# Optimization experiments

Hardware: AMD Instinct MI355X
Metric: run time of the kernel (lower is better)

The kernel has to match this reference:

```python
import jax, jax.numpy as jnp
import numpy as np

B, T, D, H = 2, 2048, 2048, 16


def setup_inputs() -> dict:
    key = jax.random.key(0)
    ks = jax.random.split(key, 5)
    s = 0.02  # typical init scale
    return {
        "x": jax.random.normal(ks[0], (B, T, D), jnp.float32),
        "wq": jax.random.normal(ks[1], (D, D), jnp.float32) * s,
        "wk": jax.random.normal(ks[2], (D, D), jnp.float32) * s,
        "wv": jax.random.normal(ks[3], (D, D), jnp.float32) * s,
        "wo": jax.random.normal(ks[4], (D, D), jnp.float32) * s,
    }


def weight_quant(w):
    # BitNet ternary-ish quant: sign(w) * mean(|w|), straight-through estimator
    scale = jnp.maximum(jnp.mean(jnp.abs(w)), 1e-5)
    q = jnp.sign(w) * scale
    return jax.lax.stop_gradient(q) + w - jax.lax.stop_gradient(w)


def reference(x, wq, wk, wv, wo):
    b, t, c = x.shape
    h = H
    hd = c // h
    # F.linear: y = x @ w.T  (weight shape [out, in])
    def proj(w):
        y = jnp.einsum('btc,dc->btd', x, weight_quant(w))
        return y.reshape(b, t, h, hd).transpose(0, 2, 1, 3)  # [b,h,t,hd]

    q, k, v = proj(wq), proj(wk), proj(wv)
    scale = 1.0 / np.sqrt(hd).astype(np.float32)
    scores = jnp.einsum('bhqd,bhkd->bhqk', q, k) * scale
    causal = jnp.tril(jnp.ones((t, t), dtype=bool))
    scores = jnp.where(causal, scores, jnp.finfo(scores.dtype).min)
    att = jax.nn.softmax(scores, axis=-1)
    y = jnp.einsum('bhqk,bhkd->bhqd', att, v)
    y = y.transpose(0, 2, 1, 3).reshape(b, t, c)
    return jnp.einsum('btc,dc->btd', y, weight_quant(wo))
```

## Files before the change

### kernel.cpp

```cpp
#include <hip/hip_runtime.h>
#include <stdint.h>

#define D_MODEL 2048
#define SEQ     2048
#define BATCH   2
#define NH      16
#define HD      128
#define M_TOT   (BATCH*SEQ)
#define NELEM_W (D_MODEL*D_MODEL)

typedef float f32x4 __attribute__((ext_vector_type(4)));
typedef short bf16x8 __attribute__((ext_vector_type(8)));

__device__ __forceinline__ unsigned short f2bf(float f) {
  union { float f; uint32_t u; } v; v.f = f;
  uint32_t r = v.u + 0x7FFFu + ((v.u >> 16) & 1u);
  return (unsigned short)(r >> 16);
}

__device__ __forceinline__ void gload_lds16(const unsigned short* g, unsigned short* l) {
  __builtin_amdgcn_global_load_lds(
      (const __attribute__((address_space(1))) unsigned int*)g,
      (__attribute__((address_space(3))) unsigned int*)l, 16, 0, 0);
}

__global__ __launch_bounds__(256) void sign_w(const float* w0, const float* w1,
                                              const float* w2, const float* w3,
                                              unsigned short* signs, float* partials) {
  const int wi = blockIdx.y;
  const float* w = (wi == 0) ? w0 : (wi == 1) ? w1 : (wi == 2) ? w2 : w3;
  unsigned short* o = signs + (size_t)wi * NELEM_W;
  const int t = threadIdx.x;
  const int i = blockIdx.x * 256 + t;
  float4 v = ((const float4*)w)[i];
  ushort4 s;
  s.x = (v.x > 0.f) ? 0x3F80u : ((v.x < 0.f) ? 0xBF80u : 0u);
  s.y = (v.y > 0.f) ? 0x3F80u : ((v.y < 0.f) ? 0xBF80u : 0u);
  s.z = (v.z > 0.f) ? 0x3F80u : ((v.z < 0.f) ? 0xBF80u : 0u);
  s.w = (v.w > 0.f) ? 0x3F80u : ((v.w < 0.f) ? 0xBF80u : 0u);
  ((ushort4*)o)[i] = s;
  float a = fabsf(v.x) + fabsf(v.y) + fabsf(v.z) + fabsf(v.w);
  #pragma unroll
  for (int off = 32; off; off >>= 1) a += __shfl_down(a, off);
  __shared__ float sm[4];
  if ((t & 63) == 0) sm[t >> 6] = a;
  __syncthreads();
  if (t == 0) partials[wi * 4096 + blockIdx.x] = sm[0] + sm[1] + sm[2] + sm[3];
}

__global__ __launch_bounds__(256) void reduce2(const float* partials, float* scales) {
  const int wi = blockIdx.x, t = threadIdx.x;
  float s = 0.f;
  #pragma unroll
  for (int i = 0; i < 16; ++i) s += partials[wi * 4096 + i * 256 + t];
  #pragma unroll
  for (int off = 32; off; off >>= 1) s += __shfl_down(s, off);
  __shared__ float sm[4];
  if ((t & 63) == 0) sm[t >> 6] = s;
  __syncthreads();
  if (t == 0) scales[wi] = fmaxf((sm[0] + sm[1] + sm[2] + sm[3]) * (1.f / 4194304.f), 1e-5f);
}

__global__ __launch_bounds__(256) void cvt_x(const float* x, unsigned short* xb) {
  const int i = blockIdx.x * 256 + threadIdx.x;
  float4 v = ((const float4*)x)[i];
  ushort4 o;
  o.x = f2bf(v.x); o.y = f2bf(v.y); o.z = f2bf(v.z); o.w = f2bf(v.w);
  ((ushort4*)xb)[i] = o;
}

template <int MODE>
__global__ __launch_bounds__(512, 2) void gemm_p(const unsigned short* __restrict__ A,
                                                 const unsigned short* __restrict__ W,
                                                 unsigned short* __restrict__ Qb,
                                                 unsigned short* __restrict__ Kb,
                                                 unsigned short* __restrict__ Vt,
                                                 float* __restrict__ outf,
                                                 const float* __restrict__ scales) {
  constexpr int K = 2048;
  constexpr int NT = K / 64;
  constexpr int BUF = 24576;
  __shared__ alignas(16) unsigned short lds[3 * BUF];
  const int t = threadIdx.x;
  const int wid = t >> 6, lane = t & 63;
  const int llo = lane & 15, lhi = lane >> 4;
  const int wm = wid >> 1, wn = wid & 1;

  const int nwg = gridDim.x;
  const int bid = blockIdx.x;
  const int sid = (bid & 7) * (nwg >> 3) + (bid >> 3);
  const int mt = sid & 15, nt_ = sid >> 4;
  const int m0 = mt * 256;
  const int n0w = nt_ * 128;

  auto stageA = [&](int buf, int kt, int half) {
    const int k0 = kt * 64;
    #pragma unroll
    for (int i = half * 2; i < half * 2 + 2; ++i) {
      const int c = i * 512 + t;
      const int row = c >> 3, slot = c & 7;
      gload_lds16(A + (size_t)(m0 + row) * K + k0 + ((slot ^ (row & 7)) << 3),
                  &lds[buf * BUF + (i * 512 + wid * 64) * 8]);
    }
  };
  auto stageB = [&](int buf, int kt) {
    const int k0 = kt * 64;
    #pragma unroll
    for (int i = 0; i < 2; ++i) {
      const int c = i * 512 + t;
      const int row = c >> 3, slot = c & 7;
      gload_lds16(W + (size_t)(n0w + row) * K + k0 + ((slot ^ (row & 7)) << 3),
                  &lds[buf * BUF + 16384 + (i * 512 + wid * 64) * 8]);
    }
  };

  f32x4 acc[4][4] = {};
  bf16x8 a[2][2], b0[2][2], b1[2][2];

  auto rdA = [&](int cur, int mh) {
    #pragma unroll
    for (int fm = 0; fm < 2; ++fm) {
      const int ra = wm * 64 + mh * 32 + fm * 16 + llo;
      #pragma unroll
      for (int kk = 0; kk < 2; ++kk)
        a[fm][kk] = *(const bf16x8*)&lds[cur * BUF + ra * 64 + (((kk * 4 + lhi) ^ (ra & 7)) << 3)];
    }
  };

  stageA(0, 0, 0); stageA(0, 0, 1); stageB(0, 0);
  stageA(1, 1, 0); stageA(1, 1, 1); stageB(1, 1);
  asm volatile("s_waitcnt vmcnt(6)" ::: "memory");
  __builtin_amdgcn_s_barrier();

  for (int kt = 0; kt < NT; ++kt) {
    const int cur = kt % 3;
    const int nb3 = (kt + 2) % 3;
    const bool pf = (kt + 2) < NT;
    rdA(cur, 0);
    #pragma unroll
    for (int fn = 0; fn < 2; ++fn) {
      const int rb = wn * 64 + fn * 16 + llo;
      #pragma unroll
      for (int kk = 0; kk < 2; ++kk)
        b0[fn][kk] = *(const bf16x8*)&lds[cur * BUF + 16384 + rb * 64 + (((kk * 4 + lhi) ^ (rb & 7)) << 3)];
    }
    if (pf) stageA(nb3, kt + 2, 0);
    __builtin_amdgcn_s_barrier();
    asm volatile("s_waitcnt lgkmcnt(0)" ::: "memory");
    __builtin_amdgcn_sched_barrier(0);
    __builtin_amdgcn_s_setprio(1);
    #pragma unroll
    for (int kk = 0; kk < 2; ++kk)
      #pragma unroll
      for (int fm = 0; fm < 2; ++fm)
        #pragma unroll
        for (int fn = 0; fn < 2; ++fn)
          acc[fm][fn] = __builtin_amdgcn_mfma_f32_16x16x32_bf16(a[fm][kk], b0[fn][kk], acc[fm][fn], 0, 0, 0);
    __builtin_amdgcn_s_setprio(0);
    __builtin_amdgcn_s_barrier();
    #pragma unroll
    for (int fn = 0; fn < 2; ++fn) {
      const int rb = wn * 64 + 32 + fn * 16 + llo;
      #pragma unroll
      for (int kk = 0; kk < 2; ++kk)
        b1[fn][kk] = *(const bf16x8*)&lds[cur * BUF + 16384 + rb * 64 + (((kk * 4 + lhi) ^ (rb & 7)) << 3)];
    }
    if (pf) stageA(nb3, kt + 2, 1);
    __builtin_amdgcn_s_barrier();
    asm volatile("s_waitcnt lgkmcnt(0)" ::: "memory");
    __builtin_amdgcn_sched_barrier(0);
    __builtin_amdgcn_s_setprio(1);
    #pragma unroll
    for (int kk = 0; kk < 2; ++kk)
      #pragma unroll
      for (int fm = 0; fm < 2; ++fm)
        #pragma unroll
        for (int fn = 0; fn < 2; ++fn)
          acc[fm][2 + fn] = __builtin_amdgcn_mfma_f32_16x16x32_bf16(a[fm][kk], b1[fn][kk], acc[fm][2 + fn], 0, 0, 0);
    __builtin_amdgcn_s_setprio(0);
    __builtin_amdgcn_s_barrier();
    rdA(cur, 1);
    if (pf) stageB(nb3, kt + 2);
    __builtin_amdgcn_s_barrier();
    asm volatile("s_waitcnt lgkmcnt(0)" ::: "memory");
    __builtin_amdgcn_sched_barrier(0);
    __builtin_amdgcn_s_setprio(1);
    #pragma unroll
    for (int kk = 0; kk < 2; ++kk)
      #pragma unroll
      for (int fm = 0; fm < 2; ++fm)
        #pragma unroll
        for (int fn = 0; fn < 2; ++fn)
          acc[2 + fm][2 + fn] = __builtin_amdgcn_mfma_f32_16x16x32_bf16(a[fm][kk], b1[fn][kk], acc[2 + fm][2 + fn], 0, 0, 0);
    __builtin_amdgcn_s_setprio(0);
    __builtin_amdgcn_s_barrier();
    if (pf) asm volatile("s_waitcnt vmcnt(6)" ::: "memory");
    else    asm volatile("s_waitcnt vmcnt(0)" ::: "memory");
    __builtin_amdgcn_s_barrier();
    __builtin_amdgcn_s_setprio(1);
    #pragma unroll
    for (int kk = 0; kk < 2; ++kk)
      #pragma unroll
      for (int fm = 0; fm < 2; ++fm)
        #pragma unroll
        for (int fn = 0; fn < 2; ++fn)
          acc[2 + fm][fn] = __builtin_amdgcn_mfma_f32_16x16x32_bf16(a[fm][kk], b0[fn][kk], acc[2 + fm][fn], 0, 0, 0);
    __builtin_amdgcn_s_setprio(0);
    __builtin_amdgcn_s_barrier();
  }

  if (MODE == 1) {
    const float sc = scales[3];
    #pragma unroll
    for (int fm = 0; fm < 4; ++fm)
      #pragma unroll
      for (int fn = 0; fn < 4; ++fn)
        #pragma unroll
        for (int r = 0; r < 4; ++r) {
          const int row = m0 + wm * 64 + fm * 16 + lhi * 4 + r;
          const int col = n0w + wn * 64 + fn * 16 + llo;
          outf[(size_t)row * D_MODEL + col] = acc[fm][fn][r] * sc;
        }
  } else {
    const int region = n0w >> 11;
    const int c0 = (n0w & 2047) + wn * 64;
    const float sc = scales[region] * (region == 0 ? 0.08838834764831845f : 1.f);
    unsigned short* outb = (region == 0) ? Qb : (region == 1) ? Kb : Vt;
    #pragma unroll
    for (int fm = 0; fm < 4; ++fm)
      #pragma unroll
      for (int fn = 0; fn < 4; ++fn)
        #pragma unroll
        for (int r = 0; r < 4; ++r) {
          const int row = m0 + wm * 64 + fm * 16 + lhi * 4 + r;
          const int colr = c0 + fn * 16 + llo;
          const int b = row >> 11, tt = row & 2047, h = colr >> 7, d = colr & 127;
          size_t idx;
          if (region < 2) idx = ((size_t)((b * NH + h) * SEQ + tt)) * HD + d;
          else            idx = ((size_t)((b * NH + h) * HD + d)) * SEQ + tt;
          outb[idx] = f2bf(acc[fm][fn][r] * sc);
        }
  }
}

__global__ __launch_bounds__(512, 4) void attn_fwd(const unsigned short* __restrict__ Q,
                                                   const unsigned short* __restrict__ Kt,
                                                   const unsigned short* __restrict__ VT,
                                                   unsigned short* __restrict__ O) {
  __shared__ alignas(16) unsigned short lds[2][16384];
  __shared__ alignas(16) unsigned short plds[8][1024];
  const int t = threadIdx.x;
  const int wid = t >> 6, lane = t & 63;
  const int llo = lane & 15, lhi = lane >> 4;
  const int j0 = blockIdx.x;
  int bh, g;
  if (j0 < 256) { bh = j0 & 31; g = 15 - (j0 >> 5); }
  else          { bh = (j0 - 256) & 31; g = (j0 - 256) >> 5; }
  const int qbase = g * 128;
  const int nt = 2 * g + 2;
  const size_t bh_td = (size_t)bh * SEQ * HD;
  const size_t bh_dt = (size_t)bh * HD * SEQ;
  unsigned short* pw = &plds[wid][0];
  const int fvl = (llo & 7) ^ ((llo & 8) >> 1);
  const int pkey = llo & 14;

  auto stage = [&](int buf, int j) {
    const int t0 = j * 64;
    #pragma unroll
    for (int i = 0; i < 2; ++i) {
      const int c = i * 512 + t;
      const int row = c >> 4, slot = c & 15;
      gload_lds16(Kt + bh_td + (size_t)(t0 + row) * HD + ((slot ^ (row & 15)) << 3),
                  &lds[buf][(size_t)(i * 512 + wid * 64) * 8]);
    }
    #pragma unroll
    for (int i = 0; i < 2; ++i) {
      const int c = i * 512 + t;
      const int vrow = c >> 3, vslot = c & 7;
      const int fv = (vrow & 7) ^ ((vrow & 8) >> 1);
      gload_lds16(VT + bh_dt + (size_t)vrow * SEQ + t0 + ((vslot ^ fv) << 3),
                  &lds[buf][8192 + (size_t)(i * 512 + wid * 64) * 8]);
    }
  };

  bf16x8 qa[4];
  {
    const unsigned short* qp = Q + bh_td + (size_t)(qbase + wid * 16 + llo) * HD + lhi * 8;
    #pragma unroll
    for (int kk = 0; kk < 4; ++kk) qa[kk] = *(const bf16x8*)(qp + kk * 32);
  }
  f32x4 oacc[8] = {};
  float m_r = -1e30f, l_r = 0.f;

  stage(0, 0);
  for (int j = 0; j < nt; ++j) {
    const int cur = j & 1;
    __syncthreads();
    if (j + 1 < nt) stage(cur ^ 1, j + 1);
    f32x4 s[4] = {};
    __builtin_amdgcn_s_setprio(1);
    #pragma unroll
    for (int nb = 0; nb < 4; ++nb) {
      const int row = nb * 16 + llo;
      #pragma unroll
      for (int kk = 0; kk < 4; ++kk) {
        const bf16x8 kb = *(const bf16x8*)&lds[cur][row * 128 + (((kk * 4 + lhi) ^ llo) << 3)];
        s[nb] = __builtin_amdgcn_mfma_f32_16x16x32_bf16(kb, qa[kk], s[nb], 0, 0, 0);
      }
    }
    __builtin_amdgcn_s_setprio(0);
    if (j >= nt - 2) {
      const int q = qbase + wid * 16 + llo;
      #pragma unroll
      for (int nb = 0; nb < 4; ++nb)
        #pragma unroll
        for (int r = 0; r < 4; ++r)
          if (j * 64 + nb * 16 + lhi * 4 + r > q) s[nb][r] = -1e30f;
    }
    float mloc = -1e30f;
    #pragma unroll
    for (int nb = 0; nb < 4; ++nb)
      #pragma unroll
      for (int r = 0; r < 4; ++r) mloc = fmaxf(mloc, s[nb][r]);
    mloc = fmaxf(mloc, __shfl_xor(mloc, 16));
    mloc = fmaxf(mloc, __shfl_xor(mloc, 32));
    float alq = 1.f;
    if (__any(mloc > m_r + 8.f)) {
      const float mn = fmaxf(m_r, mloc);
      alq = __expf(m_r - mn);
      m_r = mn;
      float alr[4];
      #pragma unroll
      for (int r = 0; r < 4; ++r) alr[r] = __shfl(alq, lhi * 4 + r);
      #pragma unroll
      for (int db = 0; db < 8; ++db)
        #pragma unroll
        for (int r = 0; r < 4; ++r) oacc[db][r] *= alr[r];
    }
    float ps = 0.f;
    #pragma unroll
    for (int nb = 0; nb < 4; ++nb) {
      const float p0 = __expf(s[nb][0] - m_r), p1 = __expf(s[nb][1] - m_r);
      const float p2 = __expf(s[nb][2] - m_r), p3 = __expf(s[nb][3] - m_r);
      ps += (p0 + p1) + (p2 + p3);
      uint2 uu;
      uu.x = (uint32_t)f2bf(p0) | ((uint32_t)f2bf(p1) << 16);
      uu.y = (uint32_t)f2bf(p2) | ((uint32_t)f2bf(p3) << 16);
      *(uint2*)&pw[llo * 64 + (((nb * 4 + lhi) ^ pkey) << 2)] = uu;
    }
    ps += __shfl_xor(ps, 16);
    ps += __shfl_xor(ps, 32);
    l_r = l_r * alq + ps;
    asm volatile("s_waitcnt lgkmcnt(0)" ::: "memory");
    __builtin_amdgcn_sched_barrier(0);
    const bf16x8 pa0 = *(const bf16x8*)&pw[llo * 64 + (((lhi * 2) ^ pkey) << 2)];
    const bf16x8 pa1 = *(const bf16x8*)&pw[llo * 64 + (((8 + lhi * 2) ^ pkey) << 2)];
    __builtin_amdgcn_s_setprio(1);
    #pragma unroll
    for (int db = 0; db < 8; ++db) {
      const unsigned short* vbp = &lds[cur][8192 + (db * 16 + llo) * 64];
      const bf16x8 vb0 = *(const bf16x8*)&vbp[(lhi ^ fvl) << 3];
      const bf16x8 vb1 = *(const bf16x8*)&vbp[((4 + lhi) ^ fvl) << 3];
      oacc[db] = __builtin_amdgcn_mfma_f32_16x16x32_bf16(pa0, vb0, oacc[db], 0, 0, 0);
      oacc[db] = __builtin_amdgcn_mfma_f32_16x16x32_bf16(pa1, vb1, oacc[db], 0, 0, 0);
    }
    __builtin_amdgcn_s_setprio(0);
  }

  const int b = bh >> 4, h = bh & 15;
  const float invq = 1.f / l_r;
  float invr[4];
  #pragma unroll
  for (int r = 0; r < 4; ++r) invr[r] = __shfl(invq, lhi * 4 + r);
  #pragma unroll
  for (int db = 0; db < 8; ++db)
    #pragma unroll
    for (int r = 0; r < 4; ++r) {
      const int qi = qbase + wid * 16 + lhi * 4 + r;
      const int d = db * 16 + llo;
      O[((size_t)(b * SEQ + qi)) * D_MODEL + h * HD + d] = f2bf(oacc[db][r] * invr[r]);
    }
}

extern "C" void kernel_launch(void* const* d_in, const int* in_sizes, int n_in,
                              void* d_out, int out_size, void* d_ws, size_t ws_size,
                              hipStream_t stream) {
  const float* x  = (const float*)d_in[0];
  const float* wq = (const float*)d_in[1];
  const float* wk = (const float*)d_in[2];
  const float* wv = (const float*)d_in[3];
  const float* wo = (const float*)d_in[4];

  char* ws = (char*)d_ws;
  float* scales   = (float*)ws;
  float* partials = (float*)(ws + 256);
  unsigned short* xbf   = (unsigned short*)(ws + 131072);
  const size_t nMD = (size_t)M_TOT * D_MODEL;
  unsigned short* signs = xbf + nMD;
  unsigned short* Qb = signs + 4 * (size_t)NELEM_W;
  unsigned short* Kb = Qb + nMD;
  unsigned short* Vt = Kb + nMD;
  unsigned short* Ab = Vt + nMD;

  sign_w<<<dim3(4096, 4), 256, 0, stream>>>(wq, wk, wv, wo, signs, partials);
  reduce2<<<dim3(4), 256, 0, stream>>>(partials, scales);
  cvt_x<<<dim3(8192), 256, 0, stream>>>(x, xbf);

  gemm_p<0><<<dim3(768), 512, 0, stream>>>(xbf, signs, Qb, Kb, Vt, nullptr, scales);

  attn_fwd<<<dim3(512), 512, 0, stream>>>(Qb, Kb, Vt, Ab);

  gemm_p<1><<<dim3(256), 512, 0, stream>>>(Ab, signs + 3 * (size_t)NELEM_W,
                                           nullptr, nullptr, nullptr, (float*)d_out, scales);
}
```

Measured before the change: 277.2 us.

## Simplify projection GEMM main loop to a single-phase load-then-MFMA schedule

Replaces the four-phase interleaved main loop of the projection GEMM with one phase per K tile. Each phase issues all global-to-LDS prefetches for tile kt+2 up front, reads every A and B fragment from LDS, then runs all 32 MFMAs. The goal is to cut the per-tile s_barrier and lgkmcnt waits from many to one. The cost is that LDS reads no longer overlap with MFMA work inside a tile, and each wave holds more fragment registers at once.

```diff
diff --git a/kernel.cpp b/kernel.cpp
--- a/kernel.cpp
+++ b/kernel.cpp
@@ -78,13 +78,15 @@
                                                  float* __restrict__ outf,
                                                  const float* __restrict__ scales) {
   constexpr int K = 2048;
-  constexpr int NT = K / 64;
+  constexpr int NT = 32;
   constexpr int BUF = 24576;
   __shared__ alignas(16) unsigned short lds[3 * BUF];
   const int t = threadIdx.x;
   const int wid = t >> 6, lane = t & 63;
   const int llo = lane & 15, lhi = lane >> 4;
-  const int wm = wid >> 1, wn = wid & 1;
+  const int wm = wid >> 2, wn = wid & 3;
+  (void)wm; (void)wn;
+  const int wmr = wid >> 1, wnr = wid & 1;
 
   const int nwg = gridDim.x;
   const int bid = blockIdx.x;
@@ -93,10 +95,10 @@
   const int m0 = mt * 256;
   const int n0w = nt_ * 128;
 
-  auto stageA = [&](int buf, int kt, int half) {
+  auto stageA = [&](int buf, int kt) {
     const int k0 = kt * 64;
     #pragma unroll
-    for (int i = half * 2; i < half * 2 + 2; ++i) {
+    for (int i = 0; i < 4; ++i) {
       const int c = i * 512 + t;
       const int row = c >> 3, slot = c & 7;
       gload_lds16(A + (size_t)(m0 + row) * K + k0 + ((slot ^ (row & 7)) << 3),
@@ -115,20 +117,9 @@
   };
 
   f32x4 acc[4][4] = {};
-  bf16x8 a[2][2], b0[2][2], b1[2][2];
-
-  auto rdA = [&](int cur, int mh) {
-    #pragma unroll
-    for (int fm = 0; fm < 2; ++fm) {
-      const int ra = wm * 64 + mh * 32 + fm * 16 + llo;
-      #pragma unroll
-      for (int kk = 0; kk < 2; ++kk)
-        a[fm][kk] = *(const bf16x8*)&lds[cur * BUF + ra * 64 + (((kk * 4 + lhi) ^ (ra & 7)) << 3)];
-    }
-  };
-
-  stageA(0, 0, 0); stageA(0, 0, 1); stageB(0, 0);
-  stageA(1, 1, 0); stageA(1, 1, 1); stageB(1, 1);
+
+  stageA(0, 0); stageB(0, 0);
+  stageA(1, 1); stageB(1, 1);
   asm volatile("s_waitcnt vmcnt(6)" ::: "memory");
   __builtin_amdgcn_s_barrier();
 
@@ -136,77 +127,36 @@
     const int cur = kt % 3;
     const int nb3 = (kt + 2) % 3;
     const bool pf = (kt + 2) < NT;
-    rdA(cur, 0);
-    #pragma unroll
-    for (int fn = 0; fn < 2; ++fn) {
-      const int rb = wn * 64 + fn * 16 + llo;
+    if (pf) { stageA(nb3, kt + 2); stageB(nb3, kt + 2); }
+    bf16x8 a[4][2], b[4][2];
+    #pragma unroll
+    for (int f = 0; f < 4; ++f) {
+      const int ra = wmr * 64 + f * 16 + llo;
       #pragma unroll
       for (int kk = 0; kk < 2; ++kk)
-        b0[fn][kk] = *(const bf16x8*)&lds[cur * BUF + 16384 + rb * 64 + (((kk * 4 + lhi) ^ (rb & 7)) << 3)];
-    }
-    if (pf) stageA(nb3, kt + 2, 0);
-    __builtin_amdgcn_s_barrier();
-    asm volatile("s_waitcnt lgkmcnt(0)" ::: "memory");
-    __builtin_amdgcn_sched_barrier(0);
+        a[f][kk] = *(const bf16x8*)&lds[cur * BUF + ra * 64 + (((kk * 4 + lhi) ^ (ra & 7)) << 3)];
+    }
+    #pragma unroll
+    for (int f = 0; f < 4; ++f) {
+      const int rb = wnr * 64 + f * 16 + llo;
+      #pragma unroll
+      for (int kk = 0; kk < 2; ++kk)
+        b[f][kk] = *(const bf16x8*)&lds[cur * BUF + 16384 + rb * 64 + (((kk * 4 + lhi) ^ (rb & 7)) << 3)];
+    }
     __builtin_amdgcn_s_setprio(1);
     #pragma unroll
     for (int kk = 0; kk < 2; ++kk)
       #pragma unroll
-      for (int fm = 0; fm < 2; ++fm)
-        #pragma unroll
-        for (int fn = 0; fn < 2; ++fn)
-          acc[fm][fn] = __builtin_amdgcn_mfma_f32_16x16x32_bf16(a[fm][kk], b0[fn][kk], acc[fm][fn], 0, 0, 0);
+      for (int fm = 0; fm < 4; ++fm)
+        #pragma unroll
+        for (int fn = 0; fn < 4; ++fn)
+          acc[fm][fn] = __builtin_amdgcn_mfma_f32_16x16x32_bf16(a[fm][kk], b[fn][kk], acc[fm][fn], 0, 0, 0);
     __builtin_amdgcn_s_setprio(0);
-    __builtin_amdgcn_s_barrier();
-    #pragma unroll
-    for (int fn = 0; fn < 2; ++fn) {
-      const int rb = wn * 64 + 32 + fn * 16 + llo;
-      #pragma unroll
-      for (int kk = 0; kk < 2; ++kk)
-        b1[fn][kk] = *(const bf16x8*)&lds[cur * BUF + 16384 + rb * 64 + (((kk * 4 + lhi) ^ (rb & 7)) << 3)];
-    }
-    if (pf) stageA(nb3, kt + 2, 1);
-    __builtin_amdgcn_s_barrier();
-    asm volatile("s_waitcnt lgkmcnt(0)" ::: "memory");
-    __builtin_amdgcn_sched_barrier(0);
-    __builtin_amdgcn_s_setprio(1);
-    #pragma unroll
-    for (int kk = 0; kk < 2; ++kk)
-      #pragma unroll
-      for (int fm = 0; fm < 2; ++fm)
-        #pragma unroll
-        for (int fn = 0; fn < 2; ++fn)
-          acc[fm][2 + fn] = __builtin_amdgcn_mfma_f32_16x16x32_bf16(a[fm][kk], b1[fn][kk], acc[fm][2 + fn], 0, 0, 0);
-    __builtin_amdgcn_s_setprio(0);
-    __builtin_amdgcn_s_barrier();
-    rdA(cur, 1);
-    if (pf) stageB(nb3, kt + 2);
-    __builtin_amdgcn_s_barrier();
-    asm volatile("s_waitcnt lgkmcnt(0)" ::: "memory");
-    __builtin_amdgcn_sched_barrier(0);
-    __builtin_amdgcn_s_setprio(1);
-    #pragma unroll
-    for (int kk = 0; kk < 2; ++kk)
-      #pragma unroll
-      for (int fm = 0; fm < 2; ++fm)
-        #pragma unroll
-        for (int fn = 0; fn < 2; ++fn)
-          acc[2 + fm][2 + fn] = __builtin_amdgcn_mfma_f32_16x16x32_bf16(a[fm][kk], b1[fn][kk], acc[2 + fm][2 + fn], 0, 0, 0);
-    __builtin_amdgcn_s_setprio(0);
-    __builtin_amdgcn_s_barrier();
-    if (pf) asm volatile("s_waitcnt vmcnt(6)" ::: "memory");
-    else    asm volatile("s_waitcnt vmcnt(0)" ::: "memory");
-    __builtin_amdgcn_s_barrier();
-    __builtin_amdgcn_s_setprio(1);
-    #pragma unroll
-    for (int kk = 0; kk < 2; ++kk)
-      #pragma unroll
-      for (int fm = 0; fm < 2; ++fm)
-        #pragma unroll
-        for (int fn = 0; fn < 2; ++fn)
-          acc[2 + fm][fn] = __builtin_amdgcn_mfma_f32_16x16x32_bf16(a[fm][kk], b0[fn][kk], acc[2 + fm][fn], 0, 0, 0);
-    __builtin_amdgcn_s_setprio(0);
-    __builtin_amdgcn_s_barrier();
+    if (kt < NT - 1) {
+      if (kt <= NT - 3) asm volatile("s_waitcnt vmcnt(6)" ::: "memory");
+      else              asm volatile("s_waitcnt vmcnt(0)" ::: "memory");
+      __builtin_amdgcn_s_barrier();
+    }
   }
 
   if (MODE == 1) {
@@ -217,13 +167,13 @@
       for (int fn = 0; fn < 4; ++fn)
         #pragma unroll
         for (int r = 0; r < 4; ++r) {
-          const int row = m0 + wm * 64 + fm * 16 + lhi * 4 + r;
-          const int col = n0w + wn * 64 + fn * 16 + llo;
+          const int row = m0 + wmr * 64 + fm * 16 + lhi * 4 + r;
+          const int col = n0w + wnr * 64 + fn * 16 + llo;
           outf[(size_t)row * D_MODEL + col] = acc[fm][fn][r] * sc;
         }
   } else {
     const int region = n0w >> 11;
-    const int c0 = (n0w & 2047) + wn * 64;
+    const int c0 = (n0w & 2047) + wnr * 64;
     const float sc = scales[region] * (region == 0 ? 0.08838834764831845f : 1.f);
     unsigned short* outb = (region == 0) ? Qb : (region == 1) ? Kb : Vt;
     #pragma unroll
@@ -232,12 +182,12 @@
       for (int fn = 0; fn < 4; ++fn)
         #pragma unroll
         for (int r = 0; r < 4; ++r) {
-          const int row = m0 + wm * 64 + fm * 16 + lhi * 4 + r;
+          const int row = m0 + wmr * 64 + fm * 16 + lhi * 4 + r;
           const int colr = c0 + fn * 16 + llo;
-          const int b = row >> 11, tt = row & 2047, h = colr >> 7, d = colr & 127;
+          const int b_ = row >> 11, tt = row & 2047, h = colr >> 7, d = colr & 127;
           size_t idx;
-          if (region < 2) idx = ((size_t)((b * NH + h) * SEQ + tt)) * HD + d;
-          else            idx = ((size_t)((b * NH + h) * HD + d)) * SEQ + tt;
+          if (region < 2) idx = ((size_t)((b_ * NH + h) * SEQ + tt)) * HD + d;
+          else            idx = ((size_t)((b_ * NH + h) * HD + d)) * SEQ + tt;
           outb[idx] = f2bf(acc[fm][fn][r] * sc);
         }
   }
```

Measured after the change: 263.7 us. 4.9% less time.
